# Performance work log

Hardware: AMD Instinct MI355X
Metric: run time of the kernel (lower is better)

## Reference

```python
import jax, jax.numpy as jnp
import numpy as np


def setup_inputs() -> dict:
    key = jax.random.key(0)
    k1, k2 = jax.random.split(key)
    x = jax.random.normal(k1, (32, 128, 56, 56), dtype=jnp.float32)
    weight = jax.random.normal(k2, (256, 128, 3, 3), dtype=jnp.float32)
    return {"x": x, "weight": weight}


def reference(x, weight):
    # Binary Weight Network forward: conv2d with sign-binarized weights (+-1),
    # stride=1, padding=0 (VALID), dilation=1, groups=1, no bias.
    w = jnp.sign(weight)
    out = jax.lax.conv_general_dilated(
        x, w,
        window_strides=(1, 1),
        padding='VALID',
        dimension_numbers=('NCHW', 'OIHW', 'NCHW'),
    )
    return out
```

## Files before the change

### kernel.cpp

```cpp
#include <hip/hip_runtime.h>
#include <hip/hip_bf16.h>
#include <hip/hip_fp16.h>


#define NB   32
#define CIN  128
#define HIN  56
#define WIN  56
#define OC   256
#define OHO  54
#define OWO  54
#define XELF ((size_t)NB * HIN * WIN * CIN)
#define ROWB (WIN * CIN * 2)

typedef _Float16 half8 __attribute__((ext_vector_type(8)));
typedef float    f32x4 __attribute__((ext_vector_type(4)));

__global__ __launch_bounds__(256) void prep_x16(const float* __restrict__ x,
                                                _Float16* __restrict__ xp) {
    const int h = blockIdx.x;
    const int n = blockIdx.y;
    __shared__ float tile[CIN * 68];

    const float* src = x + ((size_t)n * CIN * HIN + h) * WIN;
    #pragma unroll
    for (int it = 0; it < 7; ++it) {
        const int g = threadIdx.x + it * 256;
        const int c = g / 14, q = g - c * 14;
        const float4 v = *reinterpret_cast<const float4*>(
            src + (size_t)c * (HIN * WIN) + q * 4);
        *reinterpret_cast<float4*>(&tile[c * 68 + q * 4]) = v;
    }
    __syncthreads();

    _Float16* dst = xp + ((size_t)n * HIN + h) * WIN * CIN;
    #pragma unroll
    for (int it = 0; it < 4; ++it) {
        const int item = threadIdx.x + it * 256;
        if (item < 896) {
            const int w  = item >> 4;
            const int c0 = (item & 15) * 8;
            half8 o;
            #pragma unroll
            for (int i = 0; i < 8; ++i)
                o[i] = (_Float16)tile[(c0 + i) * 68 + w];
            *reinterpret_cast<half8*>(dst + (size_t)w * CIN + c0) = o;
        }
    }
}

__global__ __launch_bounds__(256) void prep_w(const float* __restrict__ w,
                                              _Float16* __restrict__ apack) {
    int t = blockIdx.x * 256 + threadIdx.x;
    if (t >= 9 * 4 * 16 * 64) return;
    int lane  = t & 63;
    int mtile = (t >> 6) & 15;
    int cstep = (t >> 10) & 3;
    int khkw  = t >> 12;
    int kh = khkw / 3, kw = khkw % 3;
    int oc = mtile * 16 + (lane & 15);
    int c0 = cstep * 32 + (lane >> 4) * 8;
    half8 buf;
    #pragma unroll
    for (int i = 0; i < 8; ++i) {
        float wv = w[(((size_t)oc * CIN + c0 + i) * 3 + kh) * 3 + kw];
        buf[i] = (_Float16)((wv > 0.f) ? 1.f : ((wv < 0.f) ? -1.f : 0.f));
    }
    *reinterpret_cast<half8*>(apack + (size_t)t * 8) = buf;
}

__global__ __launch_bounds__(256, 2) void bconv_mfma(
        const _Float16* __restrict__ xp,
        const _Float16* __restrict__ apack,
        float* __restrict__ out) {
    __shared__ alignas(16) unsigned char smem[2 * ROWB];

    const int r   = blockIdx.x;
    const int lin = (r & 7) * 108 + (r >> 3);
    const int ohp = lin % 27;
    const int n   = lin / 27;
    const int oh0 = ohp * 2;
    const int tid  = threadIdx.x;
    const int lane = tid & 63;
    const int wave = tid >> 6;
    const int col  = lane & 15;
    const int kgrp = lane >> 4;

    f32x4 acc[2][4][4];
    #pragma unroll
    for (int p = 0; p < 2; ++p)
        #pragma unroll
        for (int m = 0; m < 4; ++m)
            #pragma unroll
            for (int nt = 0; nt < 4; ++nt)
                acc[p][m][nt] = (f32x4){0.f, 0.f, 0.f, 0.f};

    const _Float16* abase = apack + ((size_t)(wave * 4) * 64 + lane) * 8;

    auto stage_sync = [&](int k) {
        const size_t rowoff = ((size_t)n * HIN + oh0 + k) * (WIN * CIN);
        #pragma unroll
        for (int it = 0; it < 4; ++it) {
            const int g = tid + it * 256;
            if (g < 896) {
                const int pos = g >> 4, gr = g & 15;
                const uint4 v = *reinterpret_cast<const uint4*>(
                    xp + rowoff + (size_t)pos * CIN + gr * 8);
                *reinterpret_cast<uint4*>(
                    smem + (k & 1) * ROWB + pos * 256 + ((gr ^ (pos & 7)) << 4)) = v;
            }
        }
    };

    stage_sync(0);
    stage_sync(1);
    __syncthreads();

    #pragma unroll
    for (int kh = 0; kh < 3; ++kh) {
        uint4 st[4];
        if (kh < 2) {
            const size_t rowoff = ((size_t)n * HIN + oh0 + kh + 2) * (WIN * CIN);
            #pragma unroll
            for (int it = 0; it < 4; ++it) {
                const int g = tid + it * 256;
                if (g < 896)
                    st[it] = *reinterpret_cast<const uint4*>(
                        xp + rowoff + (size_t)(g >> 4) * CIN + (g & 15) * 8);
            }
        }

        const int bA = (kh & 1) * ROWB;
        const int bB = ((kh + 1) & 1) * ROWB;

        #pragma unroll
        for (int kw = 0; kw < 3; ++kw) {
            const int khkw = kh * 3 + kw;
            #pragma unroll
            for (int cstep = 0; cstep < 4; ++cstep) {
                half8 a[4];
                #pragma unroll
                for (int m = 0; m < 4; ++m)
                    a[m] = *reinterpret_cast<const half8*>(
                        abase + ((size_t)(khkw * 4 + cstep) * 16 + m) * 64 * 8);

                int off[4];
                #pragma unroll
                for (int nt = 0; nt < 4; ++nt) {
                    int pos = nt * 16 + col + kw;
                    if (pos > WIN - 1) pos = WIN - 1;
                    off[nt] = pos * 256 + (((cstep * 4 + kgrp) ^ (pos & 7)) << 4);
                }

                half8 b[4];
                #pragma unroll
                for (int nt = 0; nt < 4; ++nt)
                    b[nt] = *reinterpret_cast<const half8*>(smem + bA + off[nt]);
                #pragma unroll
                for (int m = 0; m < 4; ++m)
                    #pragma unroll
                    for (int nt = 0; nt < 4; ++nt)
                        acc[0][m][nt] = __builtin_amdgcn_mfma_f32_16x16x32_f16(
                            a[m], b[nt], acc[0][m][nt], 0, 0, 0);

                #pragma unroll
                for (int nt = 0; nt < 4; ++nt)
                    b[nt] = *reinterpret_cast<const half8*>(smem + bB + off[nt]);
                #pragma unroll
                for (int m = 0; m < 4; ++m)
                    #pragma unroll
                    for (int nt = 0; nt < 4; ++nt)
                        acc[1][m][nt] = __builtin_amdgcn_mfma_f32_16x16x32_f16(
                            a[m], b[nt], acc[1][m][nt], 0, 0, 0);
            }
        }

        if (kh < 2) {
            __syncthreads();
            #pragma unroll
            for (int it = 0; it < 4; ++it) {
                const int g = tid + it * 256;
                if (g < 896)
                    *reinterpret_cast<uint4*>(
                        smem + bA + (g >> 4) * 256 + (((g & 15) ^ ((g >> 4) & 7)) << 4)) = st[it];
            }
            __syncthreads();
        }
    }

    #pragma unroll
    for (int p = 0; p < 2; ++p) {
        const int oh = oh0 + p;
        #pragma unroll
        for (int m = 0; m < 4; ++m) {
            #pragma unroll
            for (int nt = 0; nt < 4; ++nt) {
                const int ow = nt * 16 + col;
                if (ow < OWO) {
                    #pragma unroll
                    for (int j = 0; j < 4; ++j) {
                        const int oc = wave * 64 + m * 16 + kgrp * 4 + j;
                        out[(((size_t)n * OC + oc) * OHO + oh) * OWO + ow] = acc[p][m][nt][j];
                    }
                }
            }
        }
    }
}

__global__ __launch_bounds__(256) void bconv_naive(const float* __restrict__ x,
                                                   const float* __restrict__ w,
                                                   float* __restrict__ out) {
    long long idx = (long long)blockIdx.x * 256 + threadIdx.x;
    const long long total = (long long)NB * OC * OHO * OWO;
    if (idx >= total) return;
    int ow = idx % OWO; long long t = idx / OWO;
    int oh = t % OHO; t /= OHO;
    int oc = t % OC;  int n = t / OC;
    const float* xp = x + ((size_t)n * CIN * HIN + oh) * WIN + ow;
    const float* wp = w + (size_t)oc * (CIN * 9);
    float acc = 0.f;
    for (int c = 0; c < CIN; ++c) {
        #pragma unroll
        for (int kh = 0; kh < 3; ++kh)
            #pragma unroll
            for (int kw = 0; kw < 3; ++kw) {
                float wv = wp[(c * 3 + kh) * 3 + kw];
                float s = (wv > 0.f) ? 1.f : ((wv < 0.f) ? -1.f : 0.f);
                acc += s * xp[((size_t)c * HIN + kh) * WIN + kw];
            }
    }
    out[idx] = acc;
}

extern "C" void kernel_launch(void* const* d_in, const int* in_sizes, int n_in,
                              void* d_out, int out_size, void* d_ws, size_t ws_size,
                              hipStream_t stream) {
    const float* x = (const float*)d_in[0];
    const float* w = (const float*)d_in[1];
    float* out = (float*)d_out;

    const size_t WEL = (size_t)9 * 4 * 16 * 64 * 8;
    const size_t need = (XELF + WEL) * sizeof(_Float16);

    if (ws_size >= need) {
        _Float16* xp    = (_Float16*)d_ws;
        _Float16* apack = xp + XELF;

        prep_w<<<dim3(144), 256, 0, stream>>>(w, apack);
        prep_x16<<<dim3(HIN, NB), 256, 0, stream>>>(x, xp);
        bconv_mfma<<<dim3((OHO / 2) * NB), 256, 0, stream>>>(xp, apack, out);
    } else {
        const long long total = (long long)NB * OC * OHO * OWO;
        bconv_naive<<<dim3((unsigned)((total + 255) / 256)), 256, 0, stream>>>(x, w, out);
    }
}
```

Measured before the change: 212.8 us.

## Split conv MFMA blocks along output width and raise occupancy

Each conv block now covers half an output row pair (32 or 22 columns) instead of the full 54, which doubles the grid and halves accumulators and shared memory. Launch bounds go to 4 blocks per SM to use the freed registers and LDS. The prep_x16 transpose tile also moves from a padded stride of 68 with float4 stores to a stride of 57 with scalar stores, to cut bank conflicts on the column reads. The cost is that the weight fragments and the halo columns are loaded twice per row, and each loaded A fragment feeds fewer MFMAs.

```diff
diff --git a/kernel.cpp b/kernel.cpp
--- a/kernel.cpp
+++ b/kernel.cpp
@@ -10,8 +10,8 @@
 #define OC   256
 #define OHO  54
 #define OWO  54
-#define XELF ((size_t)NB * HIN * WIN * CIN)
-#define ROWB (WIN * CIN * 2)
+#define XELF  ((size_t)NB * HIN * WIN * CIN)
+#define ROWB2 (36 * 256)
 
 typedef _Float16 half8 __attribute__((ext_vector_type(8)));
 typedef float    f32x4 __attribute__((ext_vector_type(4)));
@@ -20,7 +20,7 @@
                                                 _Float16* __restrict__ xp) {
     const int h = blockIdx.x;
     const int n = blockIdx.y;
-    __shared__ float tile[CIN * 68];
+    __shared__ float tile[CIN * 57];
 
     const float* src = x + ((size_t)n * CIN * HIN + h) * WIN;
     #pragma unroll
@@ -29,7 +29,8 @@
         const int c = g / 14, q = g - c * 14;
         const float4 v = *reinterpret_cast<const float4*>(
             src + (size_t)c * (HIN * WIN) + q * 4);
-        *reinterpret_cast<float4*>(&tile[c * 68 + q * 4]) = v;
+        float* t = &tile[c * 57 + q * 4];
+        t[0] = v.x; t[1] = v.y; t[2] = v.z; t[3] = v.w;
     }
     __syncthreads();
 
@@ -43,7 +44,7 @@
             half8 o;
             #pragma unroll
             for (int i = 0; i < 8; ++i)
-                o[i] = (_Float16)tile[(c0 + i) * 68 + w];
+                o[i] = (_Float16)tile[(c0 + i) * 57 + w];
             *reinterpret_cast<half8*>(dst + (size_t)w * CIN + c0) = o;
         }
     }
@@ -69,30 +70,36 @@
     *reinterpret_cast<half8*>(apack + (size_t)t * 8) = buf;
 }
 
-__global__ __launch_bounds__(256, 2) void bconv_mfma(
+__global__ __launch_bounds__(256, 4) void bconv_mfma(
         const _Float16* __restrict__ xp,
         const _Float16* __restrict__ apack,
         float* __restrict__ out) {
-    __shared__ alignas(16) unsigned char smem[2 * ROWB];
-
-    const int r   = blockIdx.x;
-    const int lin = (r & 7) * 108 + (r >> 3);
-    const int ohp = lin % 27;
-    const int n   = lin / 27;
-    const int oh0 = ohp * 2;
+    __shared__ alignas(16) unsigned char smem[2 * ROWB2];
+
+    const int b    = blockIdx.x;
+    const int work = (b & 7) * 216 + (b >> 3);
+    const int h    = work & 1;
+    const int lin  = work >> 1;
+    const int ohp  = lin % 27;
+    const int n    = lin / 27;
+    const int oh0  = ohp * 2;
+    const int ow0  = h * 32;
+    const int pstart = h * 32;
+    const int jmax   = h ? 23 : 35;
+
     const int tid  = threadIdx.x;
     const int lane = tid & 63;
     const int wave = tid >> 6;
     const int col  = lane & 15;
     const int kgrp = lane >> 4;
 
-    f32x4 acc[2][4][4];
+    f32x4 acc[2][4][2];
     #pragma unroll
     for (int p = 0; p < 2; ++p)
         #pragma unroll
         for (int m = 0; m < 4; ++m)
             #pragma unroll
-            for (int nt = 0; nt < 4; ++nt)
+            for (int nt = 0; nt < 2; ++nt)
                 acc[p][m][nt] = (f32x4){0.f, 0.f, 0.f, 0.f};
 
     const _Float16* abase = apack + ((size_t)(wave * 4) * 64 + lane) * 8;
@@ -100,14 +107,15 @@
     auto stage_sync = [&](int k) {
         const size_t rowoff = ((size_t)n * HIN + oh0 + k) * (WIN * CIN);
         #pragma unroll
-        for (int it = 0; it < 4; ++it) {
+        for (int it = 0; it < 3; ++it) {
             const int g = tid + it * 256;
-            if (g < 896) {
-                const int pos = g >> 4, gr = g & 15;
+            if (g < 576) {
+                const int j = g >> 4, gr = g & 15;
+                int p = pstart + j; if (p > WIN - 1) p = WIN - 1;
                 const uint4 v = *reinterpret_cast<const uint4*>(
-                    xp + rowoff + (size_t)pos * CIN + gr * 8);
+                    xp + rowoff + (size_t)p * CIN + gr * 8);
                 *reinterpret_cast<uint4*>(
-                    smem + (k & 1) * ROWB + pos * 256 + ((gr ^ (pos & 7)) << 4)) = v;
+                    smem + (k & 1) * ROWB2 + j * 256 + ((gr ^ (j & 7)) << 4)) = v;
             }
         }
     };
@@ -118,20 +126,22 @@
 
     #pragma unroll
     for (int kh = 0; kh < 3; ++kh) {
-        uint4 st[4];
+        uint4 st[3];
         if (kh < 2) {
             const size_t rowoff = ((size_t)n * HIN + oh0 + kh + 2) * (WIN * CIN);
             #pragma unroll
-            for (int it = 0; it < 4; ++it) {
+            for (int it = 0; it < 3; ++it) {
                 const int g = tid + it * 256;
-                if (g < 896)
+                if (g < 576) {
+                    int p = pstart + (g >> 4); if (p > WIN - 1) p = WIN - 1;
                     st[it] = *reinterpret_cast<const uint4*>(
-                        xp + rowoff + (size_t)(g >> 4) * CIN + (g & 15) * 8);
-            }
-        }
-
-        const int bA = (kh & 1) * ROWB;
-        const int bB = ((kh + 1) & 1) * ROWB;
+                        xp + rowoff + (size_t)p * CIN + (g & 15) * 8);
+                }
+            }
+        }
+
+        const int bA = (kh & 1) * ROWB2;
+        const int bB = ((kh + 1) & 1) * ROWB2;
 
         #pragma unroll
         for (int kw = 0; kw < 3; ++kw) {
@@ -144,43 +154,43 @@
                     a[m] = *reinterpret_cast<const half8*>(
                         abase + ((size_t)(khkw * 4 + cstep) * 16 + m) * 64 * 8);
 
-                int off[4];
-                #pragma unroll
-                for (int nt = 0; nt < 4; ++nt) {
-                    int pos = nt * 16 + col + kw;
-                    if (pos > WIN - 1) pos = WIN - 1;
-                    off[nt] = pos * 256 + (((cstep * 4 + kgrp) ^ (pos & 7)) << 4);
+                int off[2];
+                #pragma unroll
+                for (int nt = 0; nt < 2; ++nt) {
+                    int j = nt * 16 + col + kw;
+                    if (j > jmax) j = jmax;
+                    off[nt] = j * 256 + (((cstep * 4 + kgrp) ^ (j & 7)) << 4);
                 }
 
-                half8 b[4];
-                #pragma unroll
-                for (int nt = 0; nt < 4; ++nt)
-                    b[nt] = *reinterpret_cast<const half8*>(smem + bA + off[nt]);
+                half8 bfrag[2];
+                #pragma unroll
+                for (int nt = 0; nt < 2; ++nt)
+                    bfrag[nt] = *reinterpret_cast<const half8*>(smem + bA + off[nt]);
                 #pragma unroll
                 for (int m = 0; m < 4; ++m)
                     #pragma unroll
-                    for (int nt = 0; nt < 4; ++nt)
+                    for (int nt = 0; nt < 2; ++nt)
                         acc[0][m][nt] = __builtin_amdgcn_mfma_f32_16x16x32_f16(
-                            a[m], b[nt], acc[0][m][nt], 0, 0, 0);
-
-                #pragma unroll
-                for (int nt = 0; nt < 4; ++nt)
-                    b[nt] = *reinterpret_cast<const half8*>(smem + bB + off[nt]);
+                            a[m], bfrag[nt], acc[0][m][nt], 0, 0, 0);
+
+                #pragma unroll
+                for (int nt = 0; nt < 2; ++nt)
+                    bfrag[nt] = *reinterpret_cast<const half8*>(smem + bB + off[nt]);
                 #pragma unroll
                 for (int m = 0; m < 4; ++m)
                     #pragma unroll
-                    for (int nt = 0; nt < 4; ++nt)
+                    for (int nt = 0; nt < 2; ++nt)
                         acc[1][m][nt] = __builtin_amdgcn_mfma_f32_16x16x32_f16(
-                            a[m], b[nt], acc[1][m][nt], 0, 0, 0);
+                            a[m], bfrag[nt], acc[1][m][nt], 0, 0, 0);
             }
         }
 
         if (kh < 2) {
             __syncthreads();
             #pragma unroll
-            for (int it = 0; it < 4; ++it) {
+            for (int it = 0; it < 3; ++it) {
                 const int g = tid + it * 256;
-                if (g < 896)
+                if (g < 576)
                     *reinterpret_cast<uint4*>(
                         smem + bA + (g >> 4) * 256 + (((g & 15) ^ ((g >> 4) & 7)) << 4)) = st[it];
             }
@@ -194,8 +204,8 @@
         #pragma unroll
         for (int m = 0; m < 4; ++m) {
             #pragma unroll
-            for (int nt = 0; nt < 4; ++nt) {
-                const int ow = nt * 16 + col;
+            for (int nt = 0; nt < 2; ++nt) {
+                const int ow = ow0 + nt * 16 + col;
                 if (ow < OWO) {
                     #pragma unroll
                     for (int j = 0; j < 4; ++j) {
@@ -217,7 +227,7 @@
     int ow = idx % OWO; long long t = idx / OWO;
     int oh = t % OHO; t /= OHO;
     int oc = t % OC;  int n = t / OC;
-    const float* xp = x + ((size_t)n * CIN * HIN + oh) * WIN + ow;
+    const float* xpp = x + ((size_t)n * CIN * HIN + oh) * WIN + ow;
     const float* wp = w + (size_t)oc * (CIN * 9);
     float acc = 0.f;
     for (int c = 0; c < CIN; ++c) {
@@ -227,7 +237,7 @@
             for (int kw = 0; kw < 3; ++kw) {
                 float wv = wp[(c * 3 + kh) * 3 + kw];
                 float s = (wv > 0.f) ? 1.f : ((wv < 0.f) ? -1.f : 0.f);
-                acc += s * xp[((size_t)c * HIN + kh) * WIN + kw];
+                acc += s * xpp[((size_t)c * HIN + kh) * WIN + kw];
             }
     }
     out[idx] = acc;
@@ -249,7 +259,7 @@
 
         prep_w<<<dim3(144), 256, 0, stream>>>(w, apack);
         prep_x16<<<dim3(HIN, NB), 256, 0, stream>>>(x, xp);
-        bconv_mfma<<<dim3((OHO / 2) * NB), 256, 0, stream>>>(xp, apack, out);
+        bconv_mfma<<<dim3(2 * (OHO / 2) * NB), 256, 0, stream>>>(xp, apack, out);
     } else {
         const long long total = (long long)NB * OC * OHO * OWO;
         bconv_naive<<<dim3((unsigned)((total + 255) / 256)), 256, 0, stream>>>(x, w, out);
```

Measured after the change: 209.5 us. About the same (-1.6%).
